# Performance work log

Hardware: AMD Instinct MI355X
Metric: run time of the kernel (lower is better)

## Reference

```python
import jax, jax.numpy as jnp
import numpy as np

N_HEADS = 8
D_K = 64
SCALE = D_K ** (-0.5)


def setup_inputs() -> dict:
    key = jax.random.key(0)
    k1, k2, k3 = jax.random.split(key, 3)
    B, C, H, W = 8, 512, 32, 32
    x = jax.random.normal(k1, (B, C, H, W), dtype=jnp.float32)
    # Linear weights stored as [in, out] so y = x @ W + b (same math as torch Linear)
    W_qkv = jax.random.normal(k2, (C, N_HEADS * D_K * 3), dtype=jnp.float32) * (1.0 / np.sqrt(C))
    b_qkv = jnp.zeros((N_HEADS * D_K * 3,), dtype=jnp.float32)
    W_out = jax.random.normal(k3, (N_HEADS * D_K, C), dtype=jnp.float32) * (1.0 / np.sqrt(N_HEADS * D_K))
    b_out = jnp.zeros((C,), dtype=jnp.float32)
    return {"x": x, "W_qkv": W_qkv, "b_qkv": b_qkv, "W_out": W_out, "b_out": b_out}


def reference(x, W_qkv, b_qkv, W_out, b_out):
    B, C, H, W = x.shape
    N = H * W
    # [B, C, H, W] -> [B, N, C]  (tokens are spatial positions)
    xf = jnp.transpose(x.reshape(B, C, N), (0, 2, 1))
    # NOTE: the original forward never applies self.norm, so neither do we.
    qkv = xf @ W_qkv + b_qkv                       # [B, N, 3*h*d]
    qkv = qkv.reshape(B, N, N_HEADS, 3 * D_K)
    q, k, v = jnp.split(qkv, 3, axis=-1)           # each [B, N, h, d]
    attn = jnp.einsum('bihd,bjhd->bijh', q, k) * SCALE
    attn = jax.nn.softmax(attn, axis=2)            # softmax over key index j
    res = jnp.einsum('bijh,bjhd->bihd', attn, v)   # [B, N, h, d]
    res = res.reshape(B, N, N_HEADS * D_K)
    res = res @ W_out + b_out
    res = res + xf                                 # residual
    res = jnp.transpose(res, (0, 2, 1)).reshape(B, C, H, W)
    return res
```

## Files before the change

### kernel.cpp

```cpp
#include <hip/hip_runtime.h>
#include <hip/hip_bf16.h>
#include <cstdint>

typedef __bf16 bf16;
typedef __attribute__((ext_vector_type(8))) __bf16 bf16x8;
typedef __attribute__((ext_vector_type(4))) __bf16 bf16x4;
typedef __attribute__((ext_vector_type(4))) float f32x4;

#define CEXP 0.1803368801111244f

__global__ __launch_bounds__(256) void prep_k(const float* __restrict__ x,
                                              const float* __restrict__ Wqkv,
                                              const float* __restrict__ Wout,
                                              bf16* __restrict__ xT,
                                              bf16* __restrict__ WqkvT,
                                              bf16* __restrict__ WoutT) {
  __shared__ bf16 t[32][33];
  const int z = blockIdx.z;
  const float* src;
  bf16* dst;
  int R, C;
  if (z < 8) {
    if (blockIdx.x >= 32) return;
    src = x + (size_t)z * 512 * 1024;
    dst = xT + (size_t)z * 1024 * 512;
    R = 512; C = 1024;
  } else if (z == 8) {
    src = Wqkv; dst = WqkvT; R = 512; C = 1536;
  } else {
    if (blockIdx.x >= 16) return;
    src = Wout; dst = WoutT; R = 512; C = 512;
  }
  const int c0 = blockIdx.x * 32, r0 = blockIdx.y * 32;
  const int tx = threadIdx.x, ty = threadIdx.y;
#pragma unroll
  for (int i = 0; i < 4; ++i)
    t[ty + i * 8][tx] = (bf16)src[(size_t)(r0 + ty + i * 8) * C + c0 + tx];
  __syncthreads();
#pragma unroll
  for (int i = 0; i < 4; ++i)
    dst[(size_t)(c0 + ty + i * 8) * R + r0 + tx] = t[tx][ty + i * 8];
}

__global__ __launch_bounds__(256) void gemm_qkv(const bf16* __restrict__ xT,
                                                const bf16* __restrict__ WqkvT,
                                                const float* __restrict__ bqkv,
                                                bf16* __restrict__ Qb,
                                                bf16* __restrict__ Kb,
                                                bf16* __restrict__ Vb) {
  __shared__ bf16 As[128 * 64];
  __shared__ bf16 Bs[128 * 64];
  const int b = blockIdx.z;
  const int m0 = blockIdx.y * 128;
  const int co0 = blockIdx.x * 128;
  const int tid = threadIdx.x;
  const int w = tid >> 6, l = tid & 63;
  const int wr = w >> 1, wc = w & 1;
  const int quad = l >> 4, l16 = l & 15;

  const bf16* A = xT + (size_t)b * 1024 * 512;

  f32x4 acc[4][4];
#pragma unroll
  for (int i = 0; i < 4; ++i)
#pragma unroll
    for (int j = 0; j < 4; ++j) acc[i][j] = (f32x4){0.f, 0.f, 0.f, 0.f};

  const int srow = w * 32 + (l >> 3);
  const int scol = (l & 7) * 8;

  for (int kk = 0; kk < 8; ++kk) {
    const int k0 = kk * 64;
    bf16x8 av[4], bv[4];
#pragma unroll
    for (int i = 0; i < 4; ++i) {
      av[i] = *(const bf16x8*)&A[(size_t)(m0 + srow + i * 8) * 512 + k0 + scol];
      bv[i] = *(const bf16x8*)&WqkvT[(size_t)(co0 + srow + i * 8) * 512 + k0 + scol];
    }
#pragma unroll
    for (int i = 0; i < 4; ++i) {
      *(bf16x8*)&As[(srow + i * 8) * 64 + scol] = av[i];
      *(bf16x8*)&Bs[(srow + i * 8) * 64 + scol] = bv[i];
    }
    __syncthreads();
#pragma unroll
    for (int ks = 0; ks < 2; ++ks) {
      bf16x8 a[4], bb[4];
#pragma unroll
      for (int rb = 0; rb < 4; ++rb)
        a[rb] = *(const bf16x8*)&As[(wr * 64 + rb * 16 + l16) * 64 + ks * 32 + quad * 8];
#pragma unroll
      for (int cb = 0; cb < 4; ++cb)
        bb[cb] = *(const bf16x8*)&Bs[(wc * 64 + cb * 16 + l16) * 64 + ks * 32 + quad * 8];
#pragma unroll
      for (int rb = 0; rb < 4; ++rb)
#pragma unroll
        for (int cb = 0; cb < 4; ++cb)
          acc[rb][cb] = __builtin_amdgcn_mfma_f32_16x16x32_bf16(a[rb], bb[cb], acc[rb][cb], 0, 0, 0);
    }
    __syncthreads();
  }

#pragma unroll
  for (int cb = 0; cb < 4; ++cb) {
    const int co = co0 + wc * 64 + cb * 16 + l16;
    const int h = co / 192;
    const int rem = co - h * 192;
    const int part = rem >> 6;
    const int dd = rem & 63;
    const float bias = bqkv[co];
    if (part == 2) {
      bf16* base = Vb + ((size_t)(b * 8 + h) * 64 + dd) * 1024;
#pragma unroll
      for (int rb = 0; rb < 4; ++rb) {
        const int n = m0 + wr * 64 + rb * 16 + quad * 4;
        f32x4 v = acc[rb][cb];
        bf16x4 ov;
#pragma unroll
        for (int r = 0; r < 4; ++r) ov[r] = (bf16)(v[r] + bias);
        *(bf16x4*)&base[n] = ov;
      }
    } else {
      const float sc = (part == 0) ? CEXP : 1.0f;
      bf16* dst = (part == 0) ? Qb : Kb;
      bf16* base = dst + ((size_t)(b * 8 + h) * 1024) * 64 + dd;
#pragma unroll
      for (int rb = 0; rb < 4; ++rb) {
        const int n = m0 + wr * 64 + rb * 16 + quad * 4;
        f32x4 v = acc[rb][cb];
#pragma unroll
        for (int r = 0; r < 4; ++r) base[(size_t)(n + r) * 64] = (bf16)((v[r] + bias) * sc);
      }
    }
  }
}

__global__ __launch_bounds__(256) void attn_k(const bf16* __restrict__ Qb,
                                              const bf16* __restrict__ Kb,
                                              const bf16* __restrict__ Vb,
                                              bf16* __restrict__ Ob) {
  __shared__ bf16 Qs[64 * 72];
  __shared__ bf16 Ks[64 * 72];
  __shared__ bf16 Vs[64 * 72];
  __shared__ bf16 Ps[64 * 72];
  const int bh = blockIdx.x;
  const int b = bh >> 3, h = bh & 7;
  const int q0 = blockIdx.y * 64;
  const int tid = threadIdx.x;
  const int w = tid >> 6, l = tid & 63;
  const int quad = l >> 4, l16 = l & 15;

  const bf16* Qg = Qb + (size_t)bh * 1024 * 64;
  const bf16* Kg = Kb + (size_t)bh * 1024 * 64;
  const bf16* Vg = Vb + (size_t)bh * 64 * 1024;

  const int r = tid >> 2, cc = (tid & 3) * 16;

  {
    bf16x8 v0 = *(const bf16x8*)&Qg[(size_t)(q0 + r) * 64 + cc];
    bf16x8 v1 = *(const bf16x8*)&Qg[(size_t)(q0 + r) * 64 + cc + 8];
    *(bf16x8*)&Qs[r * 72 + cc] = v0;
    *(bf16x8*)&Qs[r * 72 + cc + 8] = v1;
  }
  __syncthreads();
  bf16x8 aq[2];
  aq[0] = *(const bf16x8*)&Qs[(w * 16 + l16) * 72 + quad * 8];
  aq[1] = *(const bf16x8*)&Qs[(w * 16 + l16) * 72 + 32 + quad * 8];

  bf16x8 ones;
#pragma unroll
  for (int e = 0; e < 8; ++e) ones[e] = (bf16)1.0f;

  f32x4 o[4], acc_l = (f32x4){0.f, 0.f, 0.f, 0.f};
#pragma unroll
  for (int db = 0; db < 4; ++db) o[db] = (f32x4){0.f, 0.f, 0.f, 0.f};

  bf16x8 k0v = *(const bf16x8*)&Kg[(size_t)r * 64 + cc];
  bf16x8 k1v = *(const bf16x8*)&Kg[(size_t)r * 64 + cc + 8];
  bf16x8 v0v = *(const bf16x8*)&Vg[(size_t)r * 1024 + cc];
  bf16x8 v1v = *(const bf16x8*)&Vg[(size_t)r * 1024 + cc + 8];

  for (int kv = 0; kv < 16; ++kv) {
    __syncthreads();
    *(bf16x8*)&Ks[r * 72 + cc] = k0v;
    *(bf16x8*)&Ks[r * 72 + cc + 8] = k1v;
    *(bf16x8*)&Vs[r * 72 + cc] = v0v;
    *(bf16x8*)&Vs[r * 72 + cc + 8] = v1v;
    __syncthreads();
    if (kv < 15) {
      const int j0 = (kv + 1) * 64;
      k0v = *(const bf16x8*)&Kg[(size_t)(j0 + r) * 64 + cc];
      k1v = *(const bf16x8*)&Kg[(size_t)(j0 + r) * 64 + cc + 8];
      v0v = *(const bf16x8*)&Vg[(size_t)r * 1024 + j0 + cc];
      v1v = *(const bf16x8*)&Vg[(size_t)r * 1024 + j0 + cc + 8];
    }

    f32x4 s[4];
#pragma unroll
    for (int jb = 0; jb < 4; ++jb) s[jb] = (f32x4){0.f, 0.f, 0.f, 0.f};
#pragma unroll
    for (int ks = 0; ks < 2; ++ks)
#pragma unroll
      for (int jb = 0; jb < 4; ++jb) {
        bf16x8 bk = *(const bf16x8*)&Ks[(jb * 16 + l16) * 72 + ks * 32 + quad * 8];
        s[jb] = __builtin_amdgcn_mfma_f32_16x16x32_bf16(aq[ks], bk, s[jb], 0, 0, 0);
      }

#pragma unroll
    for (int jb = 0; jb < 4; ++jb)
#pragma unroll
      for (int rr = 0; rr < 4; ++rr)
        Ps[(w * 16 + quad * 4 + rr) * 72 + jb * 16 + l16] =
            (bf16)__builtin_amdgcn_exp2f(s[jb][rr]);

#pragma unroll
    for (int ks = 0; ks < 2; ++ks) {
      bf16x8 ap = *(const bf16x8*)&Ps[(w * 16 + l16) * 72 + ks * 32 + quad * 8];
      acc_l = __builtin_amdgcn_mfma_f32_16x16x32_bf16(ap, ones, acc_l, 0, 0, 0);
#pragma unroll
      for (int db = 0; db < 4; ++db) {
        bf16x8 bv = *(const bf16x8*)&Vs[(db * 16 + l16) * 72 + ks * 32 + quad * 8];
        o[db] = __builtin_amdgcn_mfma_f32_16x16x32_bf16(ap, bv, o[db], 0, 0, 0);
      }
    }
  }

  f32x4 inv;
#pragma unroll
  for (int rr = 0; rr < 4; ++rr) inv[rr] = 1.0f / acc_l[rr];
  bf16* Og = Ob + (size_t)b * 1024 * 512 + h * 64;
#pragma unroll
  for (int db = 0; db < 4; ++db)
#pragma unroll
    for (int rr = 0; rr < 4; ++rr) {
      const int n = q0 + w * 16 + quad * 4 + rr;
      Og[(size_t)n * 512 + db * 16 + l16] = (bf16)(o[db][rr] * inv[rr]);
    }
}

__global__ __launch_bounds__(256) void gemm_out(const bf16* __restrict__ Ob,
                                                const bf16* __restrict__ WoutT,
                                                const float* __restrict__ bout,
                                                const float* __restrict__ x,
                                                float* __restrict__ out) {
  __shared__ bf16 As[128 * 64];
  __shared__ bf16 Bs[128 * 64];
  const int b = blockIdx.z;
  const int m0 = blockIdx.y * 128;
  const int co0 = blockIdx.x * 128;
  const int tid = threadIdx.x;
  const int w = tid >> 6, l = tid & 63;
  const int wr = w >> 1, wc = w & 1;
  const int quad = l >> 4, l16 = l & 15;

  const bf16* A = Ob + (size_t)b * 1024 * 512;

  f32x4 acc[4][4];
#pragma unroll
  for (int i = 0; i < 4; ++i)
#pragma unroll
    for (int j = 0; j < 4; ++j) acc[i][j] = (f32x4){0.f, 0.f, 0.f, 0.f};

  const int srow = w * 32 + (l >> 3);
  const int scol = (l & 7) * 8;

  for (int kk = 0; kk < 8; ++kk) {
    const int k0 = kk * 64;
    bf16x8 av[4], bv[4];
#pragma unroll
    for (int i = 0; i < 4; ++i) {
      av[i] = *(const bf16x8*)&A[(size_t)(m0 + srow + i * 8) * 512 + k0 + scol];
      bv[i] = *(const bf16x8*)&WoutT[(size_t)(co0 + srow + i * 8) * 512 + k0 + scol];
    }
#pragma unroll
    for (int i = 0; i < 4; ++i) {
      *(bf16x8*)&As[(srow + i * 8) * 64 + scol] = av[i];
      *(bf16x8*)&Bs[(srow + i * 8) * 64 + scol] = bv[i];
    }
    __syncthreads();
#pragma unroll
    for (int ks = 0; ks < 2; ++ks) {
      bf16x8 a[4], bb[4];
#pragma unroll
      for (int rb = 0; rb < 4; ++rb)
        a[rb] = *(const bf16x8*)&As[(wr * 64 + rb * 16 + l16) * 64 + ks * 32 + quad * 8];
#pragma unroll
      for (int cb = 0; cb < 4; ++cb)
        bb[cb] = *(const bf16x8*)&Bs[(wc * 64 + cb * 16 + l16) * 64 + ks * 32 + quad * 8];
#pragma unroll
      for (int rb = 0; rb < 4; ++rb)
#pragma unroll
        for (int cb = 0; cb < 4; ++cb)
          acc[rb][cb] = __builtin_amdgcn_mfma_f32_16x16x32_bf16(a[rb], bb[cb], acc[rb][cb], 0, 0, 0);
    }
    __syncthreads();
  }

#pragma unroll
  for (int cb = 0; cb < 4; ++cb) {
    const int c = co0 + wc * 64 + cb * 16 + l16;
    const float bias = bout[c];
#pragma unroll
    for (int rb = 0; rb < 4; ++rb) {
      const int n = m0 + wr * 64 + rb * 16 + quad * 4;
      const size_t off = ((size_t)b * 512 + c) * 1024 + n;
      f32x4 res = *(const f32x4*)&x[off];
      f32x4 v = acc[rb][cb];
      f32x4 ov;
#pragma unroll
      for (int r = 0; r < 4; ++r) ov[r] = v[r] + bias + res[r];
      *(f32x4*)&out[off] = ov;
    }
  }
}

extern "C" void kernel_launch(void* const* d_in, const int* in_sizes, int n_in,
                              void* d_out, int out_size, void* d_ws, size_t ws_size,
                              hipStream_t stream) {
  const float* x = (const float*)d_in[0];
  const float* Wqkv = (const float*)d_in[1];
  const float* bqkv = (const float*)d_in[2];
  const float* Wout = (const float*)d_in[3];
  const float* bout = (const float*)d_in[4];
  float* out = (float*)d_out;
  char* ws = (char*)d_ws;

  const size_t MB = 1024 * 1024;
  bf16* xT = (bf16*)(ws);
  bf16* Ob = xT;
  bf16* Qbuf = (bf16*)(ws + 8 * MB);
  bf16* Kbuf = (bf16*)(ws + 16 * MB);
  bf16* Vbuf = (bf16*)(ws + 24 * MB);
  bf16* WqkvT = (bf16*)(ws + 32 * MB);
  bf16* WoutT = (bf16*)(ws + 32 * MB + 1572864);
  if (ws_size < 32 * MB + 1572864 + 524288) return;

  prep_k<<<dim3(48, 16, 10), dim3(32, 8), 0, stream>>>(x, Wqkv, Wout, xT, WqkvT, WoutT);
  gemm_qkv<<<dim3(12, 8, 8), 256, 0, stream>>>(xT, WqkvT, bqkv, Qbuf, Kbuf, Vbuf);
  attn_k<<<dim3(64, 16), 256, 0, stream>>>(Qbuf, Kbuf, Vbuf, Ob);
  gemm_out<<<dim3(4, 8, 8), 256, 0, stream>>>(Ob, WoutT, bout, x, out);
}
```

Baseline: 160.5 us.

## Use direct global-to-LDS loads in GEMMs and restructure attention tiling

```diff
diff --git a/kernel.cpp b/kernel.cpp
--- a/kernel.cpp
+++ b/kernel.cpp
@@ -6,6 +6,13 @@
 typedef __attribute__((ext_vector_type(8))) __bf16 bf16x8;
 typedef __attribute__((ext_vector_type(4))) __bf16 bf16x4;
 typedef __attribute__((ext_vector_type(4))) float f32x4;
+
+typedef const __attribute__((address_space(1))) void gvoid;
+typedef __attribute__((address_space(3))) void lvoid;
+
+__device__ __forceinline__ void load_lds16(const bf16* g, bf16* l) {
+  __builtin_amdgcn_global_load_lds((gvoid*)g, (lvoid*)l, 16, 0, 0);
+}
 
 #define CEXP 0.1803368801111244f
 
@@ -66,21 +73,13 @@
 #pragma unroll
     for (int j = 0; j < 4; ++j) acc[i][j] = (f32x4){0.f, 0.f, 0.f, 0.f};
 
-  const int srow = w * 32 + (l >> 3);
-  const int scol = (l & 7) * 8;
-
   for (int kk = 0; kk < 8; ++kk) {
     const int k0 = kk * 64;
-    bf16x8 av[4], bv[4];
 #pragma unroll
     for (int i = 0; i < 4; ++i) {
-      av[i] = *(const bf16x8*)&A[(size_t)(m0 + srow + i * 8) * 512 + k0 + scol];
-      bv[i] = *(const bf16x8*)&WqkvT[(size_t)(co0 + srow + i * 8) * 512 + k0 + scol];
-    }
-#pragma unroll
-    for (int i = 0; i < 4; ++i) {
-      *(bf16x8*)&As[(srow + i * 8) * 64 + scol] = av[i];
-      *(bf16x8*)&Bs[(srow + i * 8) * 64 + scol] = bv[i];
+      const int r = w * 32 + i * 8;
+      load_lds16(A + (size_t)(m0 + r + (l >> 3)) * 512 + k0 + (l & 7) * 8, &As[r * 64]);
+      load_lds16(WqkvT + (size_t)(co0 + r + (l >> 3)) * 512 + k0 + (l & 7) * 8, &Bs[r * 64]);
     }
     __syncthreads();
 #pragma unroll
@@ -139,10 +138,9 @@
                                               const bf16* __restrict__ Kb,
                                               const bf16* __restrict__ Vb,
                                               bf16* __restrict__ Ob) {
-  __shared__ bf16 Qs[64 * 72];
-  __shared__ bf16 Ks[64 * 72];
-  __shared__ bf16 Vs[64 * 72];
-  __shared__ bf16 Ps[64 * 72];
+  __shared__ bf16 Ks[128 * 72];
+  __shared__ bf16 Vs[64 * 136];
+  __shared__ bf16 PQs[64 * 136];
   const int bh = blockIdx.x;
   const int b = bh >> 3, h = bh & 7;
   const int q0 = blockIdx.y * 64;
@@ -154,18 +152,20 @@
   const bf16* Kg = Kb + (size_t)bh * 1024 * 64;
   const bf16* Vg = Vb + (size_t)bh * 64 * 1024;
 
-  const int r = tid >> 2, cc = (tid & 3) * 16;
-
   {
-    bf16x8 v0 = *(const bf16x8*)&Qg[(size_t)(q0 + r) * 64 + cc];
-    bf16x8 v1 = *(const bf16x8*)&Qg[(size_t)(q0 + r) * 64 + cc + 8];
-    *(bf16x8*)&Qs[r * 72 + cc] = v0;
-    *(bf16x8*)&Qs[r * 72 + cc + 8] = v1;
+    const int r = tid >> 2, c = (tid & 3) * 16;
+    bf16x8 v0 = *(const bf16x8*)&Qg[(size_t)(q0 + r) * 64 + c];
+    bf16x8 v1 = *(const bf16x8*)&Qg[(size_t)(q0 + r) * 64 + c + 8];
+    *(bf16x8*)&PQs[r * 72 + c] = v0;
+    *(bf16x8*)&PQs[r * 72 + c + 8] = v1;
   }
   __syncthreads();
-  bf16x8 aq[2];
-  aq[0] = *(const bf16x8*)&Qs[(w * 16 + l16) * 72 + quad * 8];
-  aq[1] = *(const bf16x8*)&Qs[(w * 16 + l16) * 72 + 32 + quad * 8];
+  bf16x8 qb[4][2];
+#pragma unroll
+  for (int nb = 0; nb < 4; ++nb)
+#pragma unroll
+    for (int ks = 0; ks < 2; ++ks)
+      qb[nb][ks] = *(const bf16x8*)&PQs[(nb * 16 + l16) * 72 + ks * 32 + quad * 8];
 
   bf16x8 ones;
 #pragma unroll
@@ -175,51 +175,69 @@
 #pragma unroll
   for (int db = 0; db < 4; ++db) o[db] = (f32x4){0.f, 0.f, 0.f, 0.f};
 
-  bf16x8 k0v = *(const bf16x8*)&Kg[(size_t)r * 64 + cc];
-  bf16x8 k1v = *(const bf16x8*)&Kg[(size_t)r * 64 + cc + 8];
-  bf16x8 v0v = *(const bf16x8*)&Vg[(size_t)r * 1024 + cc];
-  bf16x8 v1v = *(const bf16x8*)&Vg[(size_t)r * 1024 + cc + 8];
-
-  for (int kv = 0; kv < 16; ++kv) {
-    __syncthreads();
-    *(bf16x8*)&Ks[r * 72 + cc] = k0v;
-    *(bf16x8*)&Ks[r * 72 + cc + 8] = k1v;
-    *(bf16x8*)&Vs[r * 72 + cc] = v0v;
-    *(bf16x8*)&Vs[r * 72 + cc + 8] = v1v;
-    __syncthreads();
-    if (kv < 15) {
-      const int j0 = (kv + 1) * 64;
-      k0v = *(const bf16x8*)&Kg[(size_t)(j0 + r) * 64 + cc];
-      k1v = *(const bf16x8*)&Kg[(size_t)(j0 + r) * 64 + cc + 8];
-      v0v = *(const bf16x8*)&Vg[(size_t)r * 1024 + j0 + cc];
-      v1v = *(const bf16x8*)&Vg[(size_t)r * 1024 + j0 + cc + 8];
-    }
-
-    f32x4 s[4];
-#pragma unroll
-    for (int jb = 0; jb < 4; ++jb) s[jb] = (f32x4){0.f, 0.f, 0.f, 0.f};
-#pragma unroll
-    for (int ks = 0; ks < 2; ++ks)
-#pragma unroll
-      for (int jb = 0; jb < 4; ++jb) {
-        bf16x8 bk = *(const bf16x8*)&Ks[(jb * 16 + l16) * 72 + ks * 32 + quad * 8];
-        s[jb] = __builtin_amdgcn_mfma_f32_16x16x32_bf16(aq[ks], bk, s[jb], 0, 0, 0);
-      }
-
-#pragma unroll
-    for (int jb = 0; jb < 4; ++jb)
-#pragma unroll
-      for (int rr = 0; rr < 4; ++rr)
-        Ps[(w * 16 + quad * 4 + rr) * 72 + jb * 16 + l16] =
-            (bf16)__builtin_amdgcn_exp2f(s[jb][rr]);
-
+  const int kr = tid >> 1, kc = (tid & 1) * 32;
+  const int vr = tid >> 2, vc = (tid & 3) * 32;
+
+  bf16x8 ka[4], va[4];
+#pragma unroll
+  for (int e = 0; e < 4; ++e) {
+    ka[e] = *(const bf16x8*)&Kg[(size_t)kr * 64 + kc + e * 8];
+    va[e] = *(const bf16x8*)&Vg[(size_t)vr * 1024 + vc + e * 8];
+  }
+
+  for (int kv = 0; kv < 8; ++kv) {
+    __syncthreads();
+#pragma unroll
+    for (int e = 0; e < 4; ++e) {
+      *(bf16x8*)&Ks[kr * 72 + kc + e * 8] = ka[e];
+      *(bf16x8*)&Vs[vr * 136 + vc + e * 8] = va[e];
+    }
+    __syncthreads();
+    if (kv < 7) {
+      const int j0 = (kv + 1) * 128;
+#pragma unroll
+      for (int e = 0; e < 4; ++e) {
+        ka[e] = *(const bf16x8*)&Kg[(size_t)(j0 + kr) * 64 + kc + e * 8];
+        va[e] = *(const bf16x8*)&Vg[(size_t)vr * 1024 + j0 + vc + e * 8];
+      }
+    }
+
+    f32x4 s[4][2];
+#pragma unroll
+    for (int nb = 0; nb < 4; ++nb)
+#pragma unroll
+      for (int jb = 0; jb < 2; ++jb) s[nb][jb] = (f32x4){0.f, 0.f, 0.f, 0.f};
 #pragma unroll
     for (int ks = 0; ks < 2; ++ks) {
-      bf16x8 ap = *(const bf16x8*)&Ps[(w * 16 + l16) * 72 + ks * 32 + quad * 8];
+      bf16x8 kaf[2];
+#pragma unroll
+      for (int jb = 0; jb < 2; ++jb)
+        kaf[jb] = *(const bf16x8*)&Ks[(w * 32 + jb * 16 + l16) * 72 + ks * 32 + quad * 8];
+#pragma unroll
+      for (int nb = 0; nb < 4; ++nb)
+#pragma unroll
+        for (int jb = 0; jb < 2; ++jb)
+          s[nb][jb] = __builtin_amdgcn_mfma_f32_16x16x32_bf16(kaf[jb], qb[nb][ks], s[nb][jb], 0, 0, 0);
+    }
+
+#pragma unroll
+    for (int nb = 0; nb < 4; ++nb)
+#pragma unroll
+      for (int jb = 0; jb < 2; ++jb) {
+        bf16x4 pk;
+#pragma unroll
+        for (int rr = 0; rr < 4; ++rr) pk[rr] = (bf16)__builtin_amdgcn_exp2f(s[nb][jb][rr]);
+        *(bf16x4*)&PQs[(nb * 16 + l16) * 136 + w * 32 + jb * 16 + quad * 4] = pk;
+      }
+    __syncthreads();
+
+#pragma unroll
+    for (int kj = 0; kj < 4; ++kj) {
+      bf16x8 ap = *(const bf16x8*)&PQs[(w * 16 + l16) * 136 + kj * 32 + quad * 8];
       acc_l = __builtin_amdgcn_mfma_f32_16x16x32_bf16(ap, ones, acc_l, 0, 0, 0);
 #pragma unroll
       for (int db = 0; db < 4; ++db) {
-        bf16x8 bv = *(const bf16x8*)&Vs[(db * 16 + l16) * 72 + ks * 32 + quad * 8];
+        bf16x8 bv = *(const bf16x8*)&Vs[(db * 16 + l16) * 136 + kj * 32 + quad * 8];
         o[db] = __builtin_amdgcn_mfma_f32_16x16x32_bf16(ap, bv, o[db], 0, 0, 0);
       }
     }
@@ -261,21 +279,13 @@
 #pragma unroll
     for (int j = 0; j < 4; ++j) acc[i][j] = (f32x4){0.f, 0.f, 0.f, 0.f};
 
-  const int srow = w * 32 + (l >> 3);
-  const int scol = (l & 7) * 8;
-
   for (int kk = 0; kk < 8; ++kk) {
     const int k0 = kk * 64;
-    bf16x8 av[4], bv[4];
 #pragma unroll
     for (int i = 0; i < 4; ++i) {
-      av[i] = *(const bf16x8*)&A[(size_t)(m0 + srow + i * 8) * 512 + k0 + scol];
-      bv[i] = *(const bf16x8*)&WoutT[(size_t)(co0 + srow + i * 8) * 512 + k0 + scol];
-    }
-#pragma unroll
-    for (int i = 0; i < 4; ++i) {
-      *(bf16x8*)&As[(srow + i * 8) * 64 + scol] = av[i];
-      *(bf16x8*)&Bs[(srow + i * 8) * 64 + scol] = bv[i];
+      const int r = w * 32 + i * 8;
+      load_lds16(A + (size_t)(m0 + r + (l >> 3)) * 512 + k0 + (l & 7) * 8, &As[r * 64]);
+      load_lds16(WoutT + (size_t)(co0 + r + (l >> 3)) * 512 + k0 + (l & 7) * 8, &Bs[r * 64]);
     }
     __syncthreads();
 #pragma unroll
```

Result: no change. 160.5 us (+0.0%).
